# Performance work log

Hardware: AMD Instinct MI355X
Metric: run time of the kernel (lower is better)

## Reference

```python
import jax, jax.numpy as jnp
import numpy as np

F32 = jnp.float32
G_VEC = jnp.array([0.0, 0.0, -9.80665], dtype=F32)
# KITTI-style filter parameters (process / initial covariances)
COV_OMEGA = 1e-3; COV_ACC = 1e-2; COV_B_OMEGA = 6e-9; COV_B_ACC = 2e-4
COV_ROT_C_I = 1e-9; COV_T_C_I = 1e-9
COV_ROT0 = 1e-3; COV_V0 = 1e-1; COV_B_OMEGA0 = 1e-1; COV_B_ACC0 = 1e-1
COV_ROT_C_I0 = 1e-6; COV_T_C_I0 = 1e-5
Q_DIAG = jnp.array([COV_OMEGA]*3 + [COV_ACC]*3 + [COV_B_OMEGA]*3 + [COV_B_ACC]*3
                   + [COV_ROT_C_I]*3 + [COV_T_C_I]*3, dtype=F32)


def skew(x):
    z = jnp.zeros((), x.dtype)
    return jnp.stack([jnp.stack([z, -x[2], x[1]]),
                      jnp.stack([x[2], z, -x[0]]),
                      jnp.stack([-x[1], x[0], z])])


def so3exp(phi):
    I = jnp.eye(3, dtype=phi.dtype)
    angle = jnp.linalg.norm(phi)
    small = angle < 1e-8
    a = jnp.where(small, 1.0, angle)
    S = skew(phi)
    R = I + (jnp.sin(a) / a) * S + ((1.0 - jnp.cos(a)) / (a * a)) * (S @ S)
    return jnp.where(small, I + S, R)


def sen3exp(xi):
    phi = xi[:3]
    I = jnp.eye(3, dtype=xi.dtype)
    angle = jnp.linalg.norm(phi)
    small = angle < 1e-8
    a = jnp.where(small, 1.0, angle)
    S = skew(phi)
    SS = S @ S
    Rot = jnp.where(small, I + S,
                    I + (jnp.sin(a) / a) * S + ((1.0 - jnp.cos(a)) / (a * a)) * SS)
    J = jnp.where(small, I + 0.5 * S,
                  I + ((1.0 - jnp.cos(a)) / (a * a)) * S + ((a - jnp.sin(a)) / (a ** 3)) * SS)
    x = J @ xi[3:9].reshape(2, 3).T  # (3,2): columns dv, dp
    return Rot, x


def from_rpy(roll, pitch, yaw):
    c, s = jnp.cos, jnp.sin
    z = jnp.zeros((), roll.dtype); o = jnp.ones((), roll.dtype)
    Rz = jnp.stack([jnp.stack([c(yaw), -s(yaw), z]), jnp.stack([s(yaw), c(yaw), z]), jnp.stack([z, z, o])])
    Ry = jnp.stack([jnp.stack([c(pitch), z, s(pitch)]), jnp.stack([z, o, z]), jnp.stack([-s(pitch), z, c(pitch)])])
    Rx = jnp.stack([jnp.stack([o, z, z]), jnp.stack([z, c(roll), -s(roll)]), jnp.stack([z, s(roll), c(roll)])])
    return Rz @ Ry @ Rx


def _run(t, u, measurements_covs, v_mes, ang0, w_init):
    I3 = jnp.eye(3, dtype=F32)
    IdP = jnp.eye(21, dtype=F32)
    Q = jnp.diag(Q_DIAG)
    dt = t[1:] - t[:-1]
    # InitProcessCovNet.init_cov: beta = 10 ** tanh(W @ 1)
    beta = 10.0 ** jnp.tanh(w_init)
    P0 = jnp.zeros((21, 21), F32)
    I2 = jnp.eye(2, dtype=F32)
    P0 = P0.at[:2, :2].set(COV_ROT0 * beta[0] * I2)
    P0 = P0.at[3:5, 3:5].set(COV_V0 * beta[1] * I2)
    P0 = P0.at[9:12, 9:12].set(COV_B_OMEGA0 * beta[2] * I3)
    P0 = P0.at[12:15, 12:15].set(COV_B_ACC0 * beta[3] * I3)
    P0 = P0.at[15:18, 15:18].set(COV_ROT_C_I0 * beta[4] * I3)
    P0 = P0.at[18:21, 18:21].set(COV_T_C_I0 * beta[5] * I3)
    Rot0 = from_rpy(ang0[0], ang0[1], ang0[2])
    z3 = jnp.zeros(3, F32)
    state0 = (Rot0, v_mes[0], z3, z3, z3, I3, z3, P0)

    def step(carry, inp):
        Rot_p, v_p, p_p, bo_p, ba_p, Rci_p, tci_p, P = carry
        u_i, dt_i, mc_i = inp
        # ---- propagate ----
        acc = Rot_p @ (u_i[3:6] - ba_p) + G_VEC
        v = v_p + acc * dt_i
        p = p_p + v_p * dt_i + 0.5 * acc * dt_i * dt_i
        omega = (u_i[:3] - bo_p) * dt_i
        Rot = Rot_p @ so3exp(omega)
        # ---- covariance propagation ----
        vsr = skew(v_p) @ Rot_p
        psr = skew(p_p) @ Rot_p
        F = jnp.zeros((21, 21), F32)
        F = F.at[3:6, :3].set(skew(G_VEC))
        F = F.at[6:9, 3:6].set(I3)
        F = F.at[3:6, 12:15].set(-Rot_p)
        F = F.at[:3, 9:12].set(-Rot_p)
        F = F.at[3:6, 9:12].set(-vsr)
        F = F.at[6:9, 9:12].set(-psr)
        Gm = jnp.zeros((21, 18), F32)
        Gm = Gm.at[:3, :3].set(Rot_p)
        Gm = Gm.at[3:6, 3:6].set(Rot_p)
        Gm = Gm.at[3:6, :3].set(vsr)
        Gm = Gm.at[6:9, :3].set(psr)
        Gm = Gm.at[9:12, 6:9].set(I3)
        Gm = Gm.at[12:15, 9:12].set(I3)
        Gm = Gm.at[15:18, 12:15].set(I3)
        Gm = Gm.at[18:21, 15:18].set(I3)
        F = F * dt_i
        Gm = Gm * dt_i
        F2 = F @ F
        Phi = IdP + F + 0.5 * F2 + (F2 @ F) / 6.0
        P = Phi @ (P + Gm @ Q @ Gm.T) @ Phi.T
        # ---- update (zero lateral/vertical body velocity pseudo-measurement) ----
        Rot_body = Rot @ Rci_p
        v_imu = Rot.T @ v
        om = u_i[:3] - bo_p
        v_body = Rci_p.T @ v_imu + skew(tci_p) @ om
        Omega = skew(om)
        H_v_imu = Rci_p.T @ skew(v_imu)
        H_t = skew(tci_p)
        H = jnp.zeros((2, 21), F32)
        H = H.at[:, 3:6].set(Rot_body.T[1:])
        H = H.at[:, 15:18].set(H_v_imu[1:])
        H = H.at[:, 9:12].set(H_t[1:])
        H = H.at[:, 18:21].set(-Omega[1:])
        r = -v_body[1:]
        Rm = jnp.diag(mc_i)
        S = H @ P @ H.T + Rm
        K = jnp.linalg.solve(S, (P @ H.T).T).T  # (21,2)
        dx = K @ r
        dR, dxi = sen3exp(dx[:9])
        Rot_u = dR @ Rot
        v_u = dR @ v + dxi[:, 0]
        p_u = dR @ p + dxi[:, 1]
        bo_u = bo_p + dx[9:12]
        ba_u = ba_p + dx[12:15]
        Rci_u = so3exp(dx[15:18]) @ Rci_p
        tci_u = tci_p + dx[18:21]
        I_KH = IdP - K @ H
        P_u = I_KH @ P @ I_KH.T + K @ Rm @ K.T
        P_u = 0.5 * (P_u + P_u.T)
        new = (Rot_u, v_u, p_u, bo_u, ba_u, Rci_u, tci_u, P_u)
        return new, (Rot_u, v_u, p_u, bo_u, ba_u, Rci_u, tci_u)

    xs = (u[1:], dt, measurements_covs[1:])
    _, traj = jax.lax.scan(step, state0, xs)
    cat = lambda x0, xs_: jnp.concatenate([x0[None], xs_], axis=0)
    Rot = cat(Rot0, traj[0]); v = cat(state0[1], traj[1]); p = cat(state0[2], traj[2])
    bo = cat(state0[3], traj[3]); ba = cat(state0[4], traj[4])
    Rci = cat(I3, traj[5]); tci = cat(state0[6], traj[6])
    n = Rot.shape[0]
    # pack (Rot, v, p, b_omega, b_acc, Rot_c_i, t_c_i) -> [N, 30]
    return jnp.concatenate([Rot.reshape(n, 9), v, p, bo, ba, Rci.reshape(n, 9), tci], axis=1)


def setup_inputs() -> dict:
    key = jax.random.key(0)
    k1, k2, k3, k4, k5, k6 = jax.random.split(key, 6)
    N = 5000
    t = jnp.arange(N, dtype=F32) * 0.01  # 100 Hz IMU timestamps
    u = 0.1 * jax.random.normal(k1, (N, 6), dtype=F32)
    u = u.at[:, 5].add(9.80665)  # accel z ~ gravity
    measurements_covs = 0.5 * jax.random.uniform(k2, (N, 2), dtype=F32) + 0.1
    v_mes = jax.random.normal(k3, (N, 3), dtype=F32)
    p_mes = jax.random.normal(k4, (N, 3), dtype=F32)
    ang0 = 0.1 * jax.random.normal(k5, (3,), dtype=F32)
    w_init = 0.1 * jax.random.normal(k6, (6,), dtype=F32)
    return {"t": t, "u": u, "measurements_covs": measurements_covs,
            "v_mes": v_mes, "p_mes": p_mes, "ang0": ang0, "w_init": w_init, "N": N}


def reference(t, u, measurements_covs, v_mes, p_mes, ang0, w_init, N):
    # p_mes is accepted (as in run()) but unused: p[0] stays zero in init_run.
    return _run(t, u, measurements_covs, v_mes, ang0, w_init)
```

## Files before the change

### kernel.cpp

```cpp
#include <hip/hip_runtime.h>
#include <math.h>

#define GRV 9.80665f

__device__ __forceinline__ void so3coeffs(float a2, float* c1, float* c2, float* c3){
  if (a2 < 2.5e-3f){
    float a4 = a2*a2;
    *c1 = 1.f      - a2*(1.f/6.f)   + a4*(1.f/120.f);
    *c2 = 0.5f     - a2*(1.f/24.f)  + a4*(1.f/720.f);
    *c3 = (1.f/6.f)- a2*(1.f/120.f) + a4*(1.f/5040.f);
  } else {
    float a = sqrtf(a2);
    float sa = sinf(a), ca = cosf(a);
    *c1 = sa/a; *c2 = (1.f-ca)/a2; *c3 = (a-sa)/(a2*a);
  }
}

__device__ __forceinline__ void so3exp_u(float p0, float p1, float p2, float* R){
  float a2 = p0*p0+p1*p1+p2*p2;
  float c1,c2,c3; so3coeffs(a2,&c1,&c2,&c3);
  R[0]=1.f+c2*(p0*p0-a2); R[4]=1.f+c2*(p1*p1-a2); R[8]=1.f+c2*(p2*p2-a2);
  R[1]=-c1*p2+c2*p0*p1;   R[3]= c1*p2+c2*p0*p1;
  R[2]= c1*p1+c2*p0*p2;   R[6]=-c1*p1+c2*p0*p2;
  R[5]=-c1*p0+c2*p1*p2;   R[7]= c1*p0+c2*p1*p2;
}

__device__ __forceinline__ void mat3mul_u(const float* A, const float* B, float* C){
  #pragma unroll
  for (int r=0;r<3;r++)
    #pragma unroll
    for (int c=0;c<3;c++)
      C[r*3+c] = A[r*3]*B[c] + A[r*3+1]*B[3+c] + A[r*3+2]*B[6+c];
}

__device__ __forceinline__ void col_update(float* a, const float* R_, const float* n13,
                                           const float* n23, float dtv, float hdt2,
                                           float Gdt, float Ghdt2){
  float nb[9];
  #pragma unroll
  for (int jb=0;jb<3;jb++)
    nb[jb] = a[jb] - dtv*(R_[jb*3]*a[9]+R_[jb*3+1]*a[10]+R_[jb*3+2]*a[11]);
  #pragma unroll
  for (int r=0;r<3;r++){
    float s = a[3+r];
    if (r==0) s += Gdt*a[1];
    if (r==1) s -= Gdt*a[0];
    s += n13[r*3]*a[9]+n13[r*3+1]*a[10]+n13[r*3+2]*a[11];
    s -= dtv*(R_[r*3]*a[12]+R_[r*3+1]*a[13]+R_[r*3+2]*a[14]);
    nb[3+r]=s;
  }
  #pragma unroll
  for (int r=0;r<3;r++){
    float s = a[6+r];
    if (r==0) s += Ghdt2*a[1];
    if (r==1) s -= Ghdt2*a[0];
    s += dtv*a[3+r];
    s += n23[r*3]*a[9]+n23[r*3+1]*a[10]+n23[r*3+2]*a[11];
    s -= hdt2*(R_[r*3]*a[12]+R_[r*3+1]*a[13]+R_[r*3+2]*a[14]);
    nb[6+r]=s;
  }
  #pragma unroll
  for (int k=0;k<9;k++) a[k]=nb[k];
}

__global__ __launch_bounds__(128)
void iekf_kernel(const float* __restrict__ t, const float* __restrict__ u,
                 const float* __restrict__ mcov, const float* __restrict__ vmes,
                 const float* __restrict__ ang0, const float* __restrict__ winit,
                 float* __restrict__ out, int N)
{
  const int tid  = threadIdx.x;
  const int lane = tid & 63;
  const bool w0  = (tid < 64);

  __shared__ float TP[21*24];
  __shared__ float stS[36];
  __shared__ float Hb[20];
  __shared__ float PHb[44];

  float R_[9], v_[3], p_[3], bo_[3], ba_[3], Rci_[9], tci_[3];

  {
    float cr=cosf(ang0[0]), sr=sinf(ang0[0]);
    float cp=cosf(ang0[1]), sp=sinf(ang0[1]);
    float cy=cosf(ang0[2]), sy=sinf(ang0[2]);
    float Rz[9]={cy,-sy,0.f, sy,cy,0.f, 0.f,0.f,1.f};
    float Ry[9]={cp,0.f,sp, 0.f,1.f,0.f, -sp,0.f,cp};
    float Rx[9]={1.f,0.f,0.f, 0.f,cr,-sr, 0.f,sr,cr};
    float T1m[9]; mat3mul_u(Rz,Ry,T1m); mat3mul_u(T1m,Rx,R_);
  }
  v_[0]=vmes[0]; v_[1]=vmes[1]; v_[2]=vmes[2];
  #pragma unroll
  for (int k=0;k<3;k++){ p_[k]=0.f; bo_[k]=0.f; ba_[k]=0.f; tci_[k]=0.f; }
  #pragma unroll
  for (int k=0;k<9;k++) Rci_[k] = (k%4==0)?1.f:0.f;

  if (tid==0){
    ((float4*)stS)[0] = make_float4(R_[0],R_[1],R_[2],R_[3]);
    ((float4*)stS)[1] = make_float4(R_[4],R_[5],R_[6],R_[7]);
    ((float4*)stS)[2] = make_float4(R_[8],v_[0],v_[1],v_[2]);
    ((float4*)stS)[3] = make_float4(p_[0],p_[1],p_[2],bo_[0]);
    ((float4*)stS)[4] = make_float4(bo_[1],bo_[2],ba_[0],ba_[1]);
    ((float4*)stS)[5] = make_float4(ba_[2],Rci_[0],Rci_[1],Rci_[2]);
    ((float4*)stS)[6] = make_float4(Rci_[3],Rci_[4],Rci_[5],Rci_[6]);
    ((float4*)stS)[7] = make_float4(Rci_[7],Rci_[8],tci_[0],tci_[1]);
    ((float4*)stS)[8] = make_float4(tci_[2],0.f,0.f,0.f);
  }

  float creg[21], colv[21];
  #pragma unroll
  for (int j=0;j<21;j++){ creg[j]=0.f; colv[j]=0.f; }
  if (w0){
    float beta[6];
    #pragma unroll
    for (int k=0;k<6;k++) beta[k] = powf(10.f, tanhf(winit[k]));
    float dl = (lane==0||lane==1)? 1e-3f*beta[0]
             : (lane==3||lane==4)? 0.1f*beta[1]
             : (lane>=9&&lane<12)? 0.1f*beta[2]
             : (lane>=12&&lane<15)? 0.1f*beta[3]
             : (lane>=15&&lane<18)? 1e-6f*beta[4]
             : (lane>=18&&lane<21)? 1e-5f*beta[5] : 0.f;
    #pragma unroll
    for (int j=0;j<21;j++) creg[j] = (j==lane)? dl : 0.f;
    if (lane<21){
      #pragma unroll
      for (int j=0;j<21;j++) TP[j*24+lane]=creg[j];
    }
    if (lane<21){
      #pragma unroll
      for (int j=0;j<21;j++) colv[j]=TP[lane*24+j];
    }
  }

  float t_nm1 = t[0];
  float t_n   = (N>1)? t[1] : t[0];
  float mc0   = (N>1)? mcov[2] : 0.f;
  float mc1   = (N>1)? mcov[3] : 0.f;
  float u6[6] = {0,0,0,0,0,0};
  if (!w0 && N>1){
    #pragma unroll
    for (int k=0;k<6;k++) u6[k]=u[6+k];
  }

  __syncthreads();

  float h03=0,h04=0,h05=0,h09=0,h011=0,h015=0,h016=0,h017=0,h018=0,h020=0;
  float h13=0,h14=0,h15=0,h19=0,h110=0,h115=0,h116=0,h117=0,h118=0,h119=0;
  float rsh0=0, rsh1=0;
  float Rn[9], vnp[3], pnp[3];
  float ctreg[21];
  float ph0=0.f, ph1=0.f;

  for (int n=1; n<N; n++){
    const float dtv  = t_n - t_nm1;
    const float dt2  = dtv*dtv;
    const float hdt2 = 0.5f*dt2;
    const float sdt3 = dt2*dtv*(1.f/6.f);
    const float Gdt  = GRV*dtv;
    const float Ghdt2= GRV*hdt2;

    if (w0){
      {
        float4 s0=((float4*)stS)[0], s1=((float4*)stS)[1], s2=((float4*)stS)[2], s3=((float4*)stS)[3];
        R_[0]=s0.x; R_[1]=s0.y; R_[2]=s0.z; R_[3]=s0.w;
        R_[4]=s1.x; R_[5]=s1.y; R_[6]=s1.z; R_[7]=s1.w;
        R_[8]=s2.x; v_[0]=s2.y; v_[1]=s2.z; v_[2]=s2.w;
        p_[0]=s3.x; p_[1]=s3.y; p_[2]=s3.z;
      }
      float vsr[9], psr[9], n13[9], n23[9];
      #pragma unroll
      for (int c=0;c<3;c++){
        vsr[c]   = v_[1]*R_[6+c] - v_[2]*R_[3+c];
        vsr[3+c] = v_[2]*R_[c]   - v_[0]*R_[6+c];
        vsr[6+c] = v_[0]*R_[3+c] - v_[1]*R_[c];
        psr[c]   = p_[1]*R_[6+c] - p_[2]*R_[3+c];
        psr[3+c] = p_[2]*R_[c]   - p_[0]*R_[6+c];
        psr[6+c] = p_[0]*R_[3+c] - p_[1]*R_[c];
      }
      #pragma unroll
      for (int c=0;c<3;c++){
        float sg0 =  GRV*R_[3+c];
        float sg1 = -GRV*R_[c];
        n13[c]   = -dtv*vsr[c]   - hdt2*sg0;
        n13[3+c] = -dtv*vsr[3+c] - hdt2*sg1;
        n13[6+c] = -dtv*vsr[6+c];
        n23[c]   = -dtv*psr[c]   - hdt2*vsr[c]   - sdt3*sg0;
        n23[3+c] = -dtv*psr[3+c] - hdt2*vsr[3+c] - sdt3*sg1;
        n23[6+c] = -dtv*psr[6+c] - hdt2*vsr[6+c];
      }
      const float vv = v_[0]*v_[0]+v_[1]*v_[1]+v_[2]*v_[2];
      const float vp = v_[0]*p_[0]+v_[1]*p_[1]+v_[2]*p_[2];
      const float pp = p_[0]*p_[0]+p_[1]*p_[1]+p_[2]*p_[2];

      float areg[21];
      #pragma unroll
      for (int j=0;j<21;j++) areg[j] = 0.5f*(creg[j] + colv[j]);
      {
        const float qom = 1e-3f*dt2, qac = 1e-2f*dt2;
        if (lane<9){
          int bi = lane/3, r3 = lane - 3*bi;
          float vrr = (r3==0)?v_[0]:(r3==1)?v_[1]:v_[2];
          float prr = (r3==0)?p_[0]:(r3==1)?p_[1]:p_[2];
          float sv0 = (r3==0)?0.f:(r3==1)? v_[2]:-v_[1];
          float sv1 = (r3==0)?-v_[2]:(r3==1)?0.f: v_[0];
          float sv2 = (r3==0)? v_[1]:(r3==1)?-v_[0]:0.f;
          float sp0 = (r3==0)?0.f:(r3==1)? p_[2]:-p_[1];
          float sp1 = (r3==0)?-p_[2]:(r3==1)?0.f: p_[0];
          float sp2 = (r3==0)? p_[1]:(r3==1)?-p_[0]:0.f;
          if (bi==0){
            areg[r3]  += qom;
            areg[3] -= qom*sv0; areg[4] -= qom*sv1; areg[5] -= qom*sv2;
            areg[6] -= qom*sp0; areg[7] -= qom*sp1; areg[8] -= qom*sp2;
          } else if (bi==1){
            areg[0] += qom*sv0; areg[1] += qom*sv1; areg[2] += qom*sv2;
            areg[3+r3] += qom*vv + qac;
            areg[3] -= qom*vrr*v_[0]; areg[4] -= qom*vrr*v_[1]; areg[5] -= qom*vrr*v_[2];
            areg[6+r3] += qom*vp;
            areg[6] -= qom*prr*v_[0]; areg[7] -= qom*prr*v_[1]; areg[8] -= qom*prr*v_[2];
          } else {
            areg[0] += qom*sp0; areg[1] += qom*sp1; areg[2] += qom*sp2;
            areg[3+r3] += qom*vp;
            areg[3] -= qom*vrr*p_[0]; areg[4] -= qom*vrr*p_[1]; areg[5] -= qom*vrr*p_[2];
            areg[6+r3] += qom*pp;
            areg[6] -= qom*prr*p_[0]; areg[7] -= qom*prr*p_[1]; areg[8] -= qom*prr*p_[2];
          }
        }
        #pragma unroll
        for (int j=9;j<21;j++){
          float qd = (j<12)? 6e-9f : (j<15)? 2e-4f : 1e-9f;
          areg[j] += (lane==j)? qd*dt2 : 0.f;
        }
      }
      if (lane>=21){
        #pragma unroll
        for (int j=0;j<21;j++) areg[j]=0.f;
      }

      col_update(areg, R_, n13, n23, dtv, hdt2, Gdt, Ghdt2);

      if (lane<21){
        #pragma unroll
        for (int j=0;j<21;j++) TP[j*24+lane]=areg[j];
      }
      if (lane<21){
        #pragma unroll
        for (int j=0;j<21;j++) ctreg[j]=TP[lane*24+j];
      } else {
        #pragma unroll
        for (int j=0;j<21;j++) ctreg[j]=0.f;
      }

      col_update(ctreg, R_, n13, n23, dtv, hdt2, Gdt, Ghdt2);
    } else {
      if (lane<33) out[(size_t)(n-1)*33 + lane] = stS[lane];
      {
        float ub0=u6[3]-ba_[0], ub1=u6[4]-ba_[1], ub2=u6[5]-ba_[2];
        float ac0=R_[0]*ub0+R_[1]*ub1+R_[2]*ub2;
        float ac1=R_[3]*ub0+R_[4]*ub1+R_[5]*ub2;
        float ac2=R_[6]*ub0+R_[7]*ub1+R_[8]*ub2 - GRV;
        vnp[0]=v_[0]+ac0*dtv; vnp[1]=v_[1]+ac1*dtv; vnp[2]=v_[2]+ac2*dtv;
        pnp[0]=p_[0]+v_[0]*dtv+0.5f*ac0*dt2;
        pnp[1]=p_[1]+v_[1]*dtv+0.5f*ac1*dt2;
        pnp[2]=p_[2]+v_[2]*dtv+0.5f*ac2*dt2;
        float E[9]; so3exp_u((u6[0]-bo_[0])*dtv,(u6[1]-bo_[1])*dtv,(u6[2]-bo_[2])*dtv, E);
        mat3mul_u(R_, E, Rn);
      }
      {
        float Rb[9]; mat3mul_u(Rn, Rci_, Rb);
        float vi0 = Rn[0]*vnp[0]+Rn[3]*vnp[1]+Rn[6]*vnp[2];
        float vi1 = Rn[1]*vnp[0]+Rn[4]*vnp[1]+Rn[7]*vnp[2];
        float vi2 = Rn[2]*vnp[0]+Rn[5]*vnp[1]+Rn[8]*vnp[2];
        float o0 = u6[0]-bo_[0], o1 = u6[1]-bo_[1], o2 = u6[2]-bo_[2];
        h03 = Rb[1]; h04 = Rb[4]; h05 = Rb[7];
        h13 = Rb[2]; h14 = Rb[5]; h15 = Rb[8];
        h09 = tci_[2];  h011 = -tci_[0];
        h19 = -tci_[1]; h110 = tci_[0];
        h015 =  Rci_[4]*vi2 - Rci_[7]*vi1;
        h016 = -Rci_[1]*vi2 + Rci_[7]*vi0;
        h017 =  Rci_[1]*vi1 - Rci_[4]*vi0;
        h115 =  Rci_[5]*vi2 - Rci_[8]*vi1;
        h116 = -Rci_[2]*vi2 + Rci_[8]*vi0;
        h117 =  Rci_[2]*vi1 - Rci_[5]*vi0;
        h018 = -o2; h020 = o0;
        h118 =  o1; h119 = -o0;
        rsh0 = -( Rci_[1]*vi0 + Rci_[4]*vi1 + Rci_[7]*vi2 + (tci_[2]*o0 - tci_[0]*o2) );
        rsh1 = -( Rci_[2]*vi0 + Rci_[5]*vi1 + Rci_[8]*vi2 + (-tci_[1]*o0 + tci_[0]*o1) );
      }
      if (lane==0){
        ((float4*)Hb)[0] = make_float4(h03,h04,h05,h09);
        ((float4*)Hb)[1] = make_float4(h011,h015,h016,h017);
        ((float4*)Hb)[2] = make_float4(h018,h020,h13,h14);
        ((float4*)Hb)[3] = make_float4(h15,h19,h110,h115);
        ((float4*)Hb)[4] = make_float4(h116,h117,h118,h119);
      }
    }
    __syncthreads();

    if (w0){
      float4 b0=((float4*)Hb)[0], b1=((float4*)Hb)[1], b2=((float4*)Hb)[2];
      float4 b3=((float4*)Hb)[3], b4=((float4*)Hb)[4];
      h03=b0.x; h04=b0.y; h05=b0.z; h09=b0.w;
      h011=b1.x; h015=b1.y; h016=b1.z; h017=b1.w;
      h018=b2.x; h020=b2.y; h13=b2.z; h14=b2.w;
      h15=b3.x; h19=b3.y; h110=b3.z; h115=b3.w;
      h116=b4.x; h117=b4.y; h118=b4.z; h119=b4.w;
      ph0 = (((ctreg[3]*h03 + ctreg[4]*h04) + (ctreg[5]*h05 + ctreg[9]*h09)) +
             ((ctreg[11]*h011 + ctreg[15]*h015) + (ctreg[16]*h016 + ctreg[17]*h017))) +
            (ctreg[18]*h018 + ctreg[20]*h020);
      ph1 = (((ctreg[3]*h13 + ctreg[4]*h14) + (ctreg[5]*h15 + ctreg[9]*h19)) +
             ((ctreg[10]*h110 + ctreg[15]*h115) + (ctreg[16]*h116 + ctreg[17]*h117))) +
            (ctreg[18]*h118 + ctreg[19]*h119);
      if (lane<21) *(float2*)&PHb[lane*2] = make_float2(ph0, ph1);
    }
    __syncthreads();

    float pj0[21], pj1[21];
    {
      #pragma unroll
      for (int q=0;q<11;q++){
        float4 v4 = ((float4*)PHb)[q];
        if (2*q   < 21){ pj0[2*q]   = v4.x; pj1[2*q]   = v4.y; }
        if (2*q+1 < 21){ pj0[2*q+1] = v4.z; pj1[2*q+1] = v4.w; }
      }
    }
    float s00 = mc0 + ((((h03*pj0[3] + h04*pj0[4]) + (h05*pj0[5] + h09*pj0[9])) +
                        ((h011*pj0[11] + h015*pj0[15]) + (h016*pj0[16] + h017*pj0[17]))) +
                       (h018*pj0[18] + h020*pj0[20]));
    float s01 =        ((((h03*pj1[3] + h04*pj1[4]) + (h05*pj1[5] + h09*pj1[9])) +
                        ((h011*pj1[11] + h015*pj1[15]) + (h016*pj1[16] + h017*pj1[17]))) +
                       (h018*pj1[18] + h020*pj1[20]));
    float s10 =        ((((h13*pj0[3] + h14*pj0[4]) + (h15*pj0[5] + h19*pj0[9])) +
                        ((h110*pj0[10] + h115*pj0[15]) + (h116*pj0[16] + h117*pj0[17]))) +
                       (h118*pj0[18] + h119*pj0[19]));
    float s11 = mc1 + ((((h13*pj1[3] + h14*pj1[4]) + (h15*pj1[5] + h19*pj1[9])) +
                        ((h110*pj1[10] + h115*pj1[15]) + (h116*pj1[16] + h117*pj1[17]))) +
                       (h118*pj1[18] + h119*pj1[19]));
    float id  = 1.f/(s00*s11 - s01*s10);
    float i00 =  s11*id, i01 = -s01*id, i10 = -s10*id, i11 = s00*id;
    float sm01 = 0.5f*(s01+s10);

    if (w0){
      float ki0 = ph0*i00 + ph1*i10;
      float ki1 = ph0*i01 + ph1*i11;
      float ai0 = s00*ki0 + sm01*ki1;
      float ai1 = sm01*ki0 + s11*ki1;
      float al = -ki0 + (ai0 - ph0)*i00 + (ai1 - ph1)*i01;
      float be = -ki1 + (ai0 - ph0)*i10 + (ai1 - ph1)*i11;
      #pragma unroll
      for (int j=0;j<21;j++) creg[j] = ctreg[j] + al*pj0[j] + be*pj1[j];
      if (lane<21){
        #pragma unroll
        for (int j=0;j<21;j++) TP[j*24+lane]=creg[j];
      }
      if (lane<21){
        #pragma unroll
        for (int j=0;j<21;j++) colv[j]=TP[lane*24+j];
      }
    } else {
      float g0 = i00*rsh0 + i01*rsh1;
      float g1 = i10*rsh0 + i11*rsh1;
      float dx[21];
      #pragma unroll
      for (int j=0;j<21;j++) dx[j] = pj0[j]*g0 + pj1[j]*g1;
      {
        float q0=dx[0], q1=dx[1], q2=dx[2];
        float a2 = q0*q0+q1*q1+q2*q2;
        float c1,c2,c3; so3coeffs(a2,&c1,&c2,&c3);
        float dR[9], Jm[9];
        dR[0]=1.f+c2*(q0*q0-a2); dR[4]=1.f+c2*(q1*q1-a2); dR[8]=1.f+c2*(q2*q2-a2);
        dR[1]=-c1*q2+c2*q0*q1;   dR[3]= c1*q2+c2*q0*q1;
        dR[2]= c1*q1+c2*q0*q2;   dR[6]=-c1*q1+c2*q0*q2;
        dR[5]=-c1*q0+c2*q1*q2;   dR[7]= c1*q0+c2*q1*q2;
        Jm[0]=1.f+c3*(q0*q0-a2); Jm[4]=1.f+c3*(q1*q1-a2); Jm[8]=1.f+c3*(q2*q2-a2);
        Jm[1]=-c2*q2+c3*q0*q1;   Jm[3]= c2*q2+c3*q0*q1;
        Jm[2]= c2*q1+c3*q0*q2;   Jm[6]=-c2*q1+c3*q0*q2;
        Jm[5]=-c2*q0+c3*q1*q2;   Jm[7]= c2*q0+c3*q1*q2;
        float xv[3], xp[3];
        #pragma unroll
        for (int r=0;r<3;r++){
          xv[r]=Jm[r*3]*dx[3]+Jm[r*3+1]*dx[4]+Jm[r*3+2]*dx[5];
          xp[r]=Jm[r*3]*dx[6]+Jm[r*3+1]*dx[7]+Jm[r*3+2]*dx[8];
        }
        float Rn2[9]; mat3mul_u(dR, Rn, Rn2);
        #pragma unroll
        for (int r=0;r<3;r++){
          float vv2 = dR[r*3]*vnp[0]+dR[r*3+1]*vnp[1]+dR[r*3+2]*vnp[2] + xv[r];
          float pp2 = dR[r*3]*pnp[0]+dR[r*3+1]*pnp[1]+dR[r*3+2]*pnp[2] + xp[r];
          v_[r]=vv2; p_[r]=pp2;
          bo_[r]+=dx[9+r]; ba_[r]+=dx[12+r]; tci_[r]+=dx[18+r];
        }
        float E2[9]; so3exp_u(dx[15],dx[16],dx[17],E2);
        float Rc2[9]; mat3mul_u(E2, Rci_, Rc2);
        #pragma unroll
        for (int k=0;k<9;k++){ Rci_[k]=Rc2[k]; R_[k]=Rn2[k]; }
      }
      if (lane==0){
        ((float4*)stS)[0] = make_float4(R_[0],R_[1],R_[2],R_[3]);
        ((float4*)stS)[1] = make_float4(R_[4],R_[5],R_[6],R_[7]);
        ((float4*)stS)[2] = make_float4(R_[8],v_[0],v_[1],v_[2]);
        ((float4*)stS)[3] = make_float4(p_[0],p_[1],p_[2],bo_[0]);
        ((float4*)stS)[4] = make_float4(bo_[1],bo_[2],ba_[0],ba_[1]);
        ((float4*)stS)[5] = make_float4(ba_[2],Rci_[0],Rci_[1],Rci_[2]);
        ((float4*)stS)[6] = make_float4(Rci_[3],Rci_[4],Rci_[5],Rci_[6]);
        ((float4*)stS)[7] = make_float4(Rci_[7],Rci_[8],tci_[0],tci_[1]);
        ((float4*)stS)[8] = make_float4(tci_[2],0.f,0.f,0.f);
      }
    }

    {
      int np = n+1;
      t_nm1 = t_n;
      if (np < N){
        t_n = t[np];
        mc0 = mcov[np*2]; mc1 = mcov[np*2+1];
        if (!w0){
          #pragma unroll
          for (int k=0;k<6;k++) u6[k]=u[np*6+k];
        }
      }
    }
    __syncthreads();
  }

  if (!w0 && lane<33) out[(size_t)(N-1)*33 + lane] = stS[lane];
}

extern "C" void kernel_launch(void* const* d_in, const int* in_sizes, int n_in,
                              void* d_out, int out_size, void* d_ws, size_t ws_size,
                              hipStream_t stream) {
  const float* t     = (const float*)d_in[0];
  const float* u     = (const float*)d_in[1];
  const float* mcov  = (const float*)d_in[2];
  const float* vmes  = (const float*)d_in[3];
  const float* ang0  = (const float*)d_in[5];
  const float* winit = (const float*)d_in[6];
  float* out = (float*)d_out;
  int N = in_sizes[0];
  iekf_kernel<<<dim3(1), dim3(128), 0, stream>>>(t, u, mcov, vmes, ang0, winit, out, N);
}
```

Baseline: 14.25 ms.

## Duplicate second covariance pass in both warps to remove a block barrier

```diff
diff --git a/kernel.cpp b/kernel.cpp
--- a/kernel.cpp
+++ b/kernel.cpp
@@ -74,9 +74,11 @@
   const bool w0  = (tid < 64);
 
   __shared__ float TP[21*24];
+  __shared__ float TQ[21*24];
   __shared__ float stS[36];
   __shared__ float Hb[20];
-  __shared__ float PHb[44];
+  __shared__ float PHb0[44];
+  __shared__ float PHb1[44];
 
   float R_[9], v_[3], p_[3], bo_[3], ba_[3], Rci_[9], tci_[3];
 
@@ -124,11 +126,11 @@
     for (int j=0;j<21;j++) creg[j] = (j==lane)? dl : 0.f;
     if (lane<21){
       #pragma unroll
-      for (int j=0;j<21;j++) TP[j*24+lane]=creg[j];
+      for (int j=0;j<21;j++) TQ[j*24+lane]=creg[j];
     }
     if (lane<21){
       #pragma unroll
-      for (int j=0;j<21;j++) colv[j]=TP[lane*24+j];
+      for (int j=0;j<21;j++) colv[j]=TQ[lane*24+j];
     }
   }
 
@@ -148,8 +150,7 @@
   float h13=0,h14=0,h15=0,h19=0,h110=0,h115=0,h116=0,h117=0,h118=0,h119=0;
   float rsh0=0, rsh1=0;
   float Rn[9], vnp[3], pnp[3];
-  float ctreg[21];
-  float ph0=0.f, ph1=0.f;
+  float n13[9], n23[9];
 
   for (int n=1; n<N; n++){
     const float dtv  = t_n - t_nm1;
@@ -159,6 +160,18 @@
     const float Gdt  = GRV*dtv;
     const float Ghdt2= GRV*hdt2;
 
+    const int np = n+1;
+    float t_nx=t_n, mc0x=mc0, mc1x=mc1;
+    float u6x[6] = {u6[0],u6[1],u6[2],u6[3],u6[4],u6[5]};
+    if (np < N){
+      t_nx = t[np];
+      mc0x = mcov[np*2]; mc1x = mcov[np*2+1];
+      if (!w0){
+        #pragma unroll
+        for (int k=0;k<6;k++) u6x[k]=u[np*6+k];
+      }
+    }
+
     if (w0){
       {
         float4 s0=((float4*)stS)[0], s1=((float4*)stS)[1], s2=((float4*)stS)[2], s3=((float4*)stS)[3];
@@ -167,7 +180,7 @@
         R_[8]=s2.x; v_[0]=s2.y; v_[1]=s2.z; v_[2]=s2.w;
         p_[0]=s3.x; p_[1]=s3.y; p_[2]=s3.z;
       }
-      float vsr[9], psr[9], n13[9], n23[9];
+      float vsr[9], psr[9];
       #pragma unroll
       for (int c=0;c<3;c++){
         vsr[c]   = v_[1]*R_[6+c] - v_[2]*R_[3+c];
@@ -242,17 +255,31 @@
         #pragma unroll
         for (int j=0;j<21;j++) TP[j*24+lane]=areg[j];
       }
-      if (lane<21){
-        #pragma unroll
-        for (int j=0;j<21;j++) ctreg[j]=TP[lane*24+j];
-      } else {
-        #pragma unroll
-        for (int j=0;j<21;j++) ctreg[j]=0.f;
-      }
-
-      col_update(ctreg, R_, n13, n23, dtv, hdt2, Gdt, Ghdt2);
     } else {
       if (lane<33) out[(size_t)(n-1)*33 + lane] = stS[lane];
+      {
+        float vsr[9], psr[9];
+        #pragma unroll
+        for (int c=0;c<3;c++){
+          vsr[c]   = v_[1]*R_[6+c] - v_[2]*R_[3+c];
+          vsr[3+c] = v_[2]*R_[c]   - v_[0]*R_[6+c];
+          vsr[6+c] = v_[0]*R_[3+c] - v_[1]*R_[c];
+          psr[c]   = p_[1]*R_[6+c] - p_[2]*R_[3+c];
+          psr[3+c] = p_[2]*R_[c]   - p_[0]*R_[6+c];
+          psr[6+c] = p_[0]*R_[3+c] - p_[1]*R_[c];
+        }
+        #pragma unroll
+        for (int c=0;c<3;c++){
+          float sg0 =  GRV*R_[3+c];
+          float sg1 = -GRV*R_[c];
+          n13[c]   = -dtv*vsr[c]   - hdt2*sg0;
+          n13[3+c] = -dtv*vsr[3+c] - hdt2*sg1;
+          n13[6+c] = -dtv*vsr[6+c];
+          n23[c]   = -dtv*psr[c]   - hdt2*vsr[c]   - sdt3*sg0;
+          n23[3+c] = -dtv*psr[3+c] - hdt2*vsr[3+c] - sdt3*sg1;
+          n23[6+c] = -dtv*psr[6+c] - hdt2*vsr[6+c];
+        }
+      }
       {
         float ub0=u6[3]-ba_[0], ub1=u6[4]-ba_[1], ub2=u6[5]-ba_[2];
         float ac0=R_[0]*ub0+R_[1]*ub1+R_[2]*ub2;
@@ -296,6 +323,14 @@
     }
     __syncthreads();
 
+    float ctreg[21];
+    if (lane<21){
+      #pragma unroll
+      for (int j=0;j<21;j++) ctreg[j]=TP[lane*24+j];
+    } else {
+      #pragma unroll
+      for (int j=0;j<21;j++) ctreg[j]=0.f;
+    }
     if (w0){
       float4 b0=((float4*)Hb)[0], b1=((float4*)Hb)[1], b2=((float4*)Hb)[2];
       float4 b3=((float4*)Hb)[3], b4=((float4*)Hb)[4];
@@ -304,120 +339,116 @@
       h018=b2.x; h020=b2.y; h13=b2.z; h14=b2.w;
       h15=b3.x; h19=b3.y; h110=b3.z; h115=b3.w;
       h116=b4.x; h117=b4.y; h118=b4.z; h119=b4.w;
-      ph0 = (((ctreg[3]*h03 + ctreg[4]*h04) + (ctreg[5]*h05 + ctreg[9]*h09)) +
-             ((ctreg[11]*h011 + ctreg[15]*h015) + (ctreg[16]*h016 + ctreg[17]*h017))) +
-            (ctreg[18]*h018 + ctreg[20]*h020);
-      ph1 = (((ctreg[3]*h13 + ctreg[4]*h14) + (ctreg[5]*h15 + ctreg[9]*h19)) +
-             ((ctreg[10]*h110 + ctreg[15]*h115) + (ctreg[16]*h116 + ctreg[17]*h117))) +
-            (ctreg[18]*h118 + ctreg[19]*h119);
+    }
+
+    col_update(ctreg, R_, n13, n23, dtv, hdt2, Gdt, Ghdt2);
+
+    float ph0 = (((ctreg[3]*h03 + ctreg[4]*h04) + (ctreg[5]*h05 + ctreg[9]*h09)) +
+                 ((ctreg[11]*h011 + ctreg[15]*h015) + (ctreg[16]*h016 + ctreg[17]*h017))) +
+                (ctreg[18]*h018 + ctreg[20]*h020);
+    float ph1 = (((ctreg[3]*h13 + ctreg[4]*h14) + (ctreg[5]*h15 + ctreg[9]*h19)) +
+                 ((ctreg[10]*h110 + ctreg[15]*h115) + (ctreg[16]*h116 + ctreg[17]*h117))) +
+                (ctreg[18]*h118 + ctreg[19]*h119);
+    {
+      float* PHb = w0 ? PHb0 : PHb1;
       if (lane<21) *(float2*)&PHb[lane*2] = make_float2(ph0, ph1);
-    }
-    __syncthreads();
-
-    float pj0[21], pj1[21];
-    {
+      float pj0[21], pj1[21];
       #pragma unroll
       for (int q=0;q<11;q++){
         float4 v4 = ((float4*)PHb)[q];
         if (2*q   < 21){ pj0[2*q]   = v4.x; pj1[2*q]   = v4.y; }
         if (2*q+1 < 21){ pj0[2*q+1] = v4.z; pj1[2*q+1] = v4.w; }
       }
-    }
-    float s00 = mc0 + ((((h03*pj0[3] + h04*pj0[4]) + (h05*pj0[5] + h09*pj0[9])) +
-                        ((h011*pj0[11] + h015*pj0[15]) + (h016*pj0[16] + h017*pj0[17]))) +
-                       (h018*pj0[18] + h020*pj0[20]));
-    float s01 =        ((((h03*pj1[3] + h04*pj1[4]) + (h05*pj1[5] + h09*pj1[9])) +
-                        ((h011*pj1[11] + h015*pj1[15]) + (h016*pj1[16] + h017*pj1[17]))) +
-                       (h018*pj1[18] + h020*pj1[20]));
-    float s10 =        ((((h13*pj0[3] + h14*pj0[4]) + (h15*pj0[5] + h19*pj0[9])) +
-                        ((h110*pj0[10] + h115*pj0[15]) + (h116*pj0[16] + h117*pj0[17]))) +
-                       (h118*pj0[18] + h119*pj0[19]));
-    float s11 = mc1 + ((((h13*pj1[3] + h14*pj1[4]) + (h15*pj1[5] + h19*pj1[9])) +
-                        ((h110*pj1[10] + h115*pj1[15]) + (h116*pj1[16] + h117*pj1[17]))) +
-                       (h118*pj1[18] + h119*pj1[19]));
-    float id  = 1.f/(s00*s11 - s01*s10);
-    float i00 =  s11*id, i01 = -s01*id, i10 = -s10*id, i11 = s00*id;
-    float sm01 = 0.5f*(s01+s10);
-
-    if (w0){
-      float ki0 = ph0*i00 + ph1*i10;
-      float ki1 = ph0*i01 + ph1*i11;
-      float ai0 = s00*ki0 + sm01*ki1;
-      float ai1 = sm01*ki0 + s11*ki1;
-      float al = -ki0 + (ai0 - ph0)*i00 + (ai1 - ph1)*i01;
-      float be = -ki1 + (ai0 - ph0)*i10 + (ai1 - ph1)*i11;
-      #pragma unroll
-      for (int j=0;j<21;j++) creg[j] = ctreg[j] + al*pj0[j] + be*pj1[j];
-      if (lane<21){
-        #pragma unroll
-        for (int j=0;j<21;j++) TP[j*24+lane]=creg[j];
-      }
-      if (lane<21){
-        #pragma unroll
-        for (int j=0;j<21;j++) colv[j]=TP[lane*24+j];
-      }
-    } else {
-      float g0 = i00*rsh0 + i01*rsh1;
-      float g1 = i10*rsh0 + i11*rsh1;
-      float dx[21];
-      #pragma unroll
-      for (int j=0;j<21;j++) dx[j] = pj0[j]*g0 + pj1[j]*g1;
-      {
-        float q0=dx[0], q1=dx[1], q2=dx[2];
-        float a2 = q0*q0+q1*q1+q2*q2;
-        float c1,c2,c3; so3coeffs(a2,&c1,&c2,&c3);
-        float dR[9], Jm[9];
-        dR[0]=1.f+c2*(q0*q0-a2); dR[4]=1.f+c2*(q1*q1-a2); dR[8]=1.f+c2*(q2*q2-a2);
-        dR[1]=-c1*q2+c2*q0*q1;   dR[3]= c1*q2+c2*q0*q1;
-        dR[2]= c1*q1+c2*q0*q2;   dR[6]=-c1*q1+c2*q0*q2;
-        dR[5]=-c1*q0+c2*q1*q2;   dR[7]= c1*q0+c2*q1*q2;
-        Jm[0]=1.f+c3*(q0*q0-a2); Jm[4]=1.f+c3*(q1*q1-a2); Jm[8]=1.f+c3*(q2*q2-a2);
-        Jm[1]=-c2*q2+c3*q0*q1;   Jm[3]= c2*q2+c3*q0*q1;
-        Jm[2]= c2*q1+c3*q0*q2;   Jm[6]=-c2*q1+c3*q0*q2;
-        Jm[5]=-c2*q0+c3*q1*q2;   Jm[7]= c2*q0+c3*q1*q2;
-        float xv[3], xp[3];
-        #pragma unroll
-        for (int r=0;r<3;r++){
-          xv[r]=Jm[r*3]*dx[3]+Jm[r*3+1]*dx[4]+Jm[r*3+2]*dx[5];
-          xp[r]=Jm[r*3]*dx[6]+Jm[r*3+1]*dx[7]+Jm[r*3+2]*dx[8];
-        }
-        float Rn2[9]; mat3mul_u(dR, Rn, Rn2);
-        #pragma unroll
-        for (int r=0;r<3;r++){
-          float vv2 = dR[r*3]*vnp[0]+dR[r*3+1]*vnp[1]+dR[r*3+2]*vnp[2] + xv[r];
-          float pp2 = dR[r*3]*pnp[0]+dR[r*3+1]*pnp[1]+dR[r*3+2]*pnp[2] + xp[r];
-          v_[r]=vv2; p_[r]=pp2;
-          bo_[r]+=dx[9+r]; ba_[r]+=dx[12+r]; tci_[r]+=dx[18+r];
-        }
-        float E2[9]; so3exp_u(dx[15],dx[16],dx[17],E2);
-        float Rc2[9]; mat3mul_u(E2, Rci_, Rc2);
-        #pragma unroll
-        for (int k=0;k<9;k++){ Rci_[k]=Rc2[k]; R_[k]=Rn2[k]; }
-      }
-      if (lane==0){
-        ((float4*)stS)[0] = make_float4(R_[0],R_[1],R_[2],R_[3]);
-        ((float4*)stS)[1] = make_float4(R_[4],R_[5],R_[6],R_[7]);
-        ((float4*)stS)[2] = make_float4(R_[8],v_[0],v_[1],v_[2]);
-        ((float4*)stS)[3] = make_float4(p_[0],p_[1],p_[2],bo_[0]);
-        ((float4*)stS)[4] = make_float4(bo_[1],bo_[2],ba_[0],ba_[1]);
-        ((float4*)stS)[5] = make_float4(ba_[2],Rci_[0],Rci_[1],Rci_[2]);
-        ((float4*)stS)[6] = make_float4(Rci_[3],Rci_[4],Rci_[5],Rci_[6]);
-        ((float4*)stS)[7] = make_float4(Rci_[7],Rci_[8],tci_[0],tci_[1]);
-        ((float4*)stS)[8] = make_float4(tci_[2],0.f,0.f,0.f);
-      }
-    }
-
-    {
-      int np = n+1;
-      t_nm1 = t_n;
-      if (np < N){
-        t_n = t[np];
-        mc0 = mcov[np*2]; mc1 = mcov[np*2+1];
-        if (!w0){
+
+      float s00 = mc0 + ((((h03*pj0[3] + h04*pj0[4]) + (h05*pj0[5] + h09*pj0[9])) +
+                          ((h011*pj0[11] + h015*pj0[15]) + (h016*pj0[16] + h017*pj0[17]))) +
+                         (h018*pj0[18] + h020*pj0[20]));
+      float s01 =        ((((h03*pj1[3] + h04*pj1[4]) + (h05*pj1[5] + h09*pj1[9])) +
+                          ((h011*pj1[11] + h015*pj1[15]) + (h016*pj1[16] + h017*pj1[17]))) +
+                         (h018*pj1[18] + h020*pj1[20]));
+      float s10 =        ((((h13*pj0[3] + h14*pj0[4]) + (h15*pj0[5] + h19*pj0[9])) +
+                          ((h110*pj0[10] + h115*pj0[15]) + (h116*pj0[16] + h117*pj0[17]))) +
+                         (h118*pj0[18] + h119*pj0[19]));
+      float s11 = mc1 + ((((h13*pj1[3] + h14*pj1[4]) + (h15*pj1[5] + h19*pj1[9])) +
+                          ((h110*pj1[10] + h115*pj1[15]) + (h116*pj1[16] + h117*pj1[17]))) +
+                         (h118*pj1[18] + h119*pj1[19]));
+      float id  = 1.f/(s00*s11 - s01*s10);
+      float i00 =  s11*id, i01 = -s01*id, i10 = -s10*id, i11 = s00*id;
+      float sm01 = 0.5f*(s01+s10);
+
+      if (w0){
+        float ki0 = ph0*i00 + ph1*i10;
+        float ki1 = ph0*i01 + ph1*i11;
+        float ai0 = s00*ki0 + sm01*ki1;
+        float ai1 = sm01*ki0 + s11*ki1;
+        float al = -ki0 + (ai0 - ph0)*i00 + (ai1 - ph1)*i01;
+        float be = -ki1 + (ai0 - ph0)*i10 + (ai1 - ph1)*i11;
+        #pragma unroll
+        for (int j=0;j<21;j++) creg[j] = ctreg[j] + al*pj0[j] + be*pj1[j];
+        if (lane<21){
           #pragma unroll
-          for (int k=0;k<6;k++) u6[k]=u[np*6+k];
-        }
-      }
+          for (int j=0;j<21;j++) TQ[j*24+lane]=creg[j];
+        }
+        if (lane<21){
+          #pragma unroll
+          for (int j=0;j<21;j++) colv[j]=TQ[lane*24+j];
+        }
+      } else {
+        float g0 = i00*rsh0 + i01*rsh1;
+        float g1 = i10*rsh0 + i11*rsh1;
+        float dx[21];
+        #pragma unroll
+        for (int j=0;j<21;j++) dx[j] = pj0[j]*g0 + pj1[j]*g1;
+        {
+          float q0=dx[0], q1=dx[1], q2=dx[2];
+          float a2 = q0*q0+q1*q1+q2*q2;
+          float c1,c2,c3; so3coeffs(a2,&c1,&c2,&c3);
+          float dR[9], Jm[9];
+          dR[0]=1.f+c2*(q0*q0-a2); dR[4]=1.f+c2*(q1*q1-a2); dR[8]=1.f+c2*(q2*q2-a2);
+          dR[1]=-c1*q2+c2*q0*q1;   dR[3]= c1*q2+c2*q0*q1;
+          dR[2]= c1*q1+c2*q0*q2;   dR[6]=-c1*q1+c2*q0*q2;
+          dR[5]=-c1*q0+c2*q1*q2;   dR[7]= c1*q0+c2*q1*q2;
+          Jm[0]=1.f+c3*(q0*q0-a2); Jm[4]=1.f+c3*(q1*q1-a2); Jm[8]=1.f+c3*(q2*q2-a2);
+          Jm[1]=-c2*q2+c3*q0*q1;   Jm[3]= c2*q2+c3*q0*q1;
+          Jm[2]= c2*q1+c3*q0*q2;   Jm[6]=-c2*q1+c3*q0*q2;
+          Jm[5]=-c2*q0+c3*q1*q2;   Jm[7]= c2*q0+c3*q1*q2;
+          float xv[3], xp[3];
+          #pragma unroll
+          for (int r=0;r<3;r++){
+            xv[r]=Jm[r*3]*dx[3]+Jm[r*3+1]*dx[4]+Jm[r*3+2]*dx[5];
+            xp[r]=Jm[r*3]*dx[6]+Jm[r*3+1]*dx[7]+Jm[r*3+2]*dx[8];
+          }
+          float Rn2[9]; mat3mul_u(dR, Rn, Rn2);
+          #pragma unroll
+          for (int r=0;r<3;r++){
+            float vv2 = dR[r*3]*vnp[0]+dR[r*3+1]*vnp[1]+dR[r*3+2]*vnp[2] + xv[r];
+            float pp2 = dR[r*3]*pnp[0]+dR[r*3+1]*pnp[1]+dR[r*3+2]*pnp[2] + xp[r];
+            v_[r]=vv2; p_[r]=pp2;
+            bo_[r]+=dx[9+r]; ba_[r]+=dx[12+r]; tci_[r]+=dx[18+r];
+          }
+          float E2[9]; so3exp_u(dx[15],dx[16],dx[17],E2);
+          float Rc2[9]; mat3mul_u(E2, Rci_, Rc2);
+          #pragma unroll
+          for (int k=0;k<9;k++){ Rci_[k]=Rc2[k]; R_[k]=Rn2[k]; }
+        }
+        if (lane==0){
+          ((float4*)stS)[0] = make_float4(R_[0],R_[1],R_[2],R_[3]);
+          ((float4*)stS)[1] = make_float4(R_[4],R_[5],R_[6],R_[7]);
+          ((float4*)stS)[2] = make_float4(R_[8],v_[0],v_[1],v_[2]);
+          ((float4*)stS)[3] = make_float4(p_[0],p_[1],p_[2],bo_[0]);
+          ((float4*)stS)[4] = make_float4(bo_[1],bo_[2],ba_[0],ba_[1]);
+          ((float4*)stS)[5] = make_float4(ba_[2],Rci_[0],Rci_[1],Rci_[2]);
+          ((float4*)stS)[6] = make_float4(Rci_[3],Rci_[4],Rci_[5],Rci_[6]);
+          ((float4*)stS)[7] = make_float4(Rci_[7],Rci_[8],tci_[0],tci_[1]);
+          ((float4*)stS)[8] = make_float4(tci_[2],0.f,0.f,0.f);
+        }
+      }
+    }
+
+    t_nm1 = t_n; t_n = t_nx; mc0 = mc0x; mc1 = mc1x;
+    if (!w0){
+      #pragma unroll
+      for (int k=0;k<6;k++) u6[k]=u6x[k];
     }
     __syncthreads();
   }
```

Measured after the change: 13.76 ms. 3.5% less time.
